# Optimization experiments

Measured on AMD Instinct MI355X. Metric: run time of the kernel, lower is better.

The kernel has to match this reference:

```python
import jax, jax.numpy as jnp
import numpy as np

N = 50000      # nodes (both x and t sets)
D = 128        # d_hidden
E = 1600000    # edges per edge_index (avg degree 32)
LN_EPS = 1e-5


def _gin(x_src, x_dst, edge, W1, b1, W2, b2):
    # PyG GINConv, eps=0: nn(x_dst + sum_{j->i} x_src[j])
    agg = jax.ops.segment_sum(x_src[edge[0]], edge[1], num_segments=x_dst.shape[0])
    h = x_dst + agg
    h = jax.nn.relu(h @ W1 + b1)
    return h @ W2 + b2


def _layernorm(h, g, b):
    m = jnp.mean(h, axis=-1, keepdims=True)
    v = jnp.var(h, axis=-1, keepdims=True)
    return (h - m) / jnp.sqrt(v + LN_EPS) * g + b


def setup_inputs() -> dict:
    key = jax.random.key(0)
    ks = jax.random.split(key, 24)
    s = 1.0 / np.sqrt(D)
    w = lambda k: (jax.random.uniform(k, (D, D), dtype=jnp.float32) * 2 - 1) * s
    b = lambda k: (jax.random.uniform(k, (D,), dtype=jnp.float32) * 2 - 1) * s
    return {
        "x": jax.random.normal(ks[0], (N, D), dtype=jnp.float32),
        "t": jax.random.normal(ks[1], (N, D), dtype=jnp.float32),
        "e_t": jax.random.randint(ks[2], (2, E), 0, N),
        "e_xct": jax.random.randint(ks[3], (2, E), 0, N),
        # gat_tt GIN MLP
        "W1a": w(ks[4]), "b1a": b(ks[5]), "W2a": w(ks[6]), "b2a": b(ks[7]),
        # gat_xct GIN MLP
        "W1b": w(ks[8]), "b1b": b(ks[9]), "W2b": w(ks[10]), "b2b": b(ks[11]),
        # out: Linear -> ReLU -> LayerNorm
        "Wo": w(ks[12]), "bo": b(ks[13]),
        "ln_g": jnp.ones((D,), dtype=jnp.float32),
        "ln_b": jnp.zeros((D,), dtype=jnp.float32),
        # fc_x: Linear -> ReLU -> Linear
        "Wf1": w(ks[14]), "bf1": b(ks[15]), "Wf2": w(ks[16]), "bf2": b(ks[17]),
    }


def reference(x, t, e_t, e_xct,
              W1a, b1a, W2a, b2a,
              W1b, b1b, W2b, b2b,
              Wo, bo, ln_g, ln_b,
              Wf1, bf1, Wf2, bf2):
    # t = (t + gat_tt(t, e_t) + gat_xct((x, t), e_xct)).relu()
    t2 = jax.nn.relu(t
                     + _gin(t, t, e_t, W1a, b1a, W2a, b2a)
                     + _gin(x, t, e_xct, W1b, b1b, W2b, b2b))
    # out branch: Linear -> ReLU -> LayerNorm, residual add
    t_out = t2 + _layernorm(jax.nn.relu(t2 @ Wo + bo), ln_g, ln_b)
    # fc_x branch: Linear -> ReLU -> Linear, residual add
    x_out = x + (jax.nn.relu(x @ Wf1 + bf1) @ Wf2 + bf2)
    return (x_out, t_out)
```

## Files before the change

kernel.cpp:

```cpp
#include <hip/hip_runtime.h>

#define DD 128
#define BSH 7
#define LSTR 136

typedef __attribute__((ext_vector_type(8))) short bf16x8;
typedef __attribute__((ext_vector_type(4))) float f32x4;
typedef __attribute__((ext_vector_type(2))) float f32x2;

__device__ __forceinline__ unsigned short f2b(float f){
  unsigned u = __builtin_bit_cast(unsigned, f);
  u += 0x7FFFu + ((u >> 16) & 1u);
  return (unsigned short)(u >> 16);
}
__device__ __forceinline__ float blo(unsigned u){ return __builtin_bit_cast(float, u << 16); }
__device__ __forceinline__ float bhi(unsigned u){ return __builtin_bit_cast(float, u & 0xFFFF0000u); }
__device__ __forceinline__ float b2f(unsigned short h){ return __builtin_bit_cast(float, ((unsigned)h) << 16); }
__device__ __forceinline__ unsigned pk2(float a, float b){
  return (unsigned)f2b(a) | ((unsigned)f2b(b) << 16);
}

struct WP { const float* w[7]; };
__global__ __launch_bounds__(256) void k_pre(const float* __restrict__ x,
    const float* __restrict__ t, unsigned* __restrict__ xh, unsigned* __restrict__ th,
    int M, WP p, unsigned short* __restrict__ wt,
    const int* __restrict__ e_t, const int* __restrict__ e_xct,
    int* __restrict__ gbcount, int E, int NBper, int ncv, int N){
  const int bid = blockIdx.x;
  if (bid < ncv){
    int tid = bid*256 + threadIdx.x;
    if (tid < M){
      float4 v = ((const float4*)x)[tid];
      ((uint2*)xh)[tid] = make_uint2(pk2(v.x, v.y), pk2(v.z, v.w));
    } else if (tid < 2*M){
      int k = tid - M;
      float4 v = ((const float4*)t)[k];
      ((uint2*)th)[k] = make_uint2(pk2(v.x, v.y), pk2(v.z, v.w));
    }
    return;
  }
  if (bid < ncv + 7){
    const float* W = p.w[bid - ncv];
    unsigned short* dst = wt + (size_t)(bid - ncv)*DD*DD;
    for (int e = threadIdx.x; e < DD*DD; e += 256){
      int k = e >> 7, c = e & 127;
      dst[(c*DD + k) ^ ((c & 7) << 3)] = f2b(W[e]);
    }
    return;
  }
  if (bid == ncv + 7){
    const int tid = threadIdx.x;
    uint4 z; z.x = 0; z.y = 0; z.z = 0; z.w = 0;
    if (tid < 16)      ((uint4*)(xh + (size_t)N*(DD/2)))[tid]      = z;
    else if (tid < 32) ((uint4*)(th + (size_t)N*(DD/2)))[tid - 16] = z;
    return;
  }
  __shared__ int h[800];
  const int vb = bid - ncv - 8;
  const int NB2 = 2*NBper;
  for (int i = threadIdx.x; i < NB2; i += 256) h[i] = 0;
  __syncthreads();
  const long total = 2L*E;
  for (long idx = (long)vb*256 + threadIdx.x; idx < total; idx += 65536L){
    int s = idx >= E;
    int e = (int)(idx - (s ? (long)E : 0));
    int d = (s ? e_xct : e_t)[E + e];
    atomicAdd(&h[s*NBper + (d >> BSH)], 1);
  }
  __syncthreads();
  for (int i = threadIdx.x; i < NB2; i += 256)
    if (h[i]) atomicAdd(&gbcount[i], h[i]);
}

__global__ void k_bscan(const int* __restrict__ gbcount, int* __restrict__ gbase,
                        int* __restrict__ gcursor, int NB2, int total){
  __shared__ int sm[1024];
  const int t = threadIdx.x;
  int v = (t < NB2) ? gbcount[t] : 0;
  sm[t] = v; __syncthreads();
  for (int d = 1; d < 1024; d <<= 1){
    int u = (t >= d) ? sm[t-d] : 0;
    __syncthreads();
    sm[t] += u;
    __syncthreads();
  }
  if (t < NB2){ int ex = sm[t] - v; gbase[t] = ex; gcursor[t] = ex; }
  if (t == 0) gbase[NB2] = total;
}

#define SCCH 8192
__global__ __launch_bounds__(256) void k_scatter(const int* __restrict__ e_t,
    const int* __restrict__ e_xct, int* __restrict__ gcursor,
    unsigned* __restrict__ gbucket, int E, int NBper){
  __shared__ int cnt[800]; __shared__ int gpos[800]; __shared__ int cur[800];
  const int NB2 = 2*NBper;
  const int t = threadIdx.x;
  for (int i = t; i < NB2; i += 256){ cnt[i] = 0; cur[i] = 0; }
  __syncthreads();
  const long base = (long)blockIdx.x * SCCH;
  const long end  = min(base + SCCH, 2L*E);
  for (long idx = base + t; idx < end; idx += 256){
    int s = idx >= E;
    int e = (int)(idx - (s ? (long)E : 0));
    int d = (s ? e_xct : e_t)[E + e];
    atomicAdd(&cnt[s*NBper + (d >> BSH)], 1);
  }
  __syncthreads();
  for (int i = t; i < NB2; i += 256)
    if (cnt[i]) gpos[i] = atomicAdd(&gcursor[i], cnt[i]);
  __syncthreads();
  for (long idx = base + t; idx < end; idx += 256){
    int s = idx >= E;
    int e = (int)(idx - (s ? (long)E : 0));
    const int* ei = s ? e_xct : e_t;
    int sv = ei[e];
    int d  = ei[E + e];
    int b  = s*NBper + (d >> BSH);
    int pos = atomicAdd(&cur[b], 1);
    gbucket[gpos[b] + pos] = (unsigned)sv | ((unsigned)d << 16);
  }
}

__global__ __launch_bounds__(256) void k_build(const unsigned* __restrict__ gbucket,
    const int* __restrict__ gbase, int* __restrict__ offs,
    unsigned short* __restrict__ csr, int N, int E, int NBper){
  __shared__ int cnt[128]; __shared__ int pre[128]; __shared__ int cur[128];
  const int b  = blockIdx.x;
  const int s  = b >= NBper;
  const int bb = b - s*NBper;
  const int d0 = bb << BSH;
  const int t  = threadIdx.x;
  if (t < 128) cnt[t] = 0;
  __syncthreads();
  const int g0 = gbase[b], g1 = gbase[b+1];
  for (int j = g0 + t; j < g1; j += 256){
    unsigned en = gbucket[j];
    atomicAdd(&cnt[(en >> 16) & 127], 1);
  }
  __syncthreads();
  int v = (t < 128) ? cnt[t] : 0;
  if (t < 128) pre[t] = v;
  __syncthreads();
  for (int d = 1; d < 128; d <<= 1){
    int u = (t >= d && t < 128) ? pre[t-d] : 0;
    __syncthreads();
    if (t < 128) pre[t] += u;
    __syncthreads();
  }
  if (t < 128){
    int ex = pre[t] - v;
    cur[t] = ex;
    int dd = d0 + t;
    if (dd < N) offs[(size_t)s*(N+1) + dd] = (g0 - s*E) + ex;
  }
  if (t == 128 + 0 && bb == NBper-1) offs[(size_t)s*(N+1) + N] = E;
  __syncthreads();
  for (int j = g0 + t; j < g1; j += 256){
    unsigned en = gbucket[j];
    int d7 = (en >> 16) & 127;
    int pos = atomicAdd(&cur[d7], 1);
    csr[(size_t)g0 + pos] = (unsigned short)(en & 0xFFFFu);
  }
}

__global__ __launch_bounds__(256) void k_gather(const unsigned short* __restrict__ th,
    const unsigned short* __restrict__ xh, const int* __restrict__ offs,
    const unsigned short* __restrict__ csr, unsigned short* hA, unsigned short* hB,
    int N, int E){
  const int w = threadIdx.x >> 6, l = threadIdx.x & 63;
  const long wid = (long)blockIdx.x*4 + w;
  if (wid >= 2L*N) return;
  const int s = wid >= N;
  const int i = (int)(wid - (s ? N : 0));
  const int* off = offs + (size_t)s*(N+1);
  const unsigned short* src = s ? xh : th;
  const unsigned short* cs = csr + (size_t)s*E;
  const int o0 = off[i], o1 = off[i+1];
  const int deg = o1 - o0;
  const int rs = l >> 4;
  const int q  = l & 15;
  const unsigned short* srcq = src + q*8;
  f32x2 A0 = 0.f, A1 = 0.f, A2 = 0.f, A3 = 0.f;
  if (deg > 0){
    int ce = cs[o0 + (l < deg ? l : deg-1)];
    for (int base = 0; base < deg; base += 64){
      const int nb = min(64, deg - base);
      const int ce_cur = ce;
      const int nxt = base + 64;
      if (nxt < deg){
        const int rem2 = deg - nxt;
        ce = cs[o0 + nxt + (l < rem2 ? l : rem2-1)];
      }
      for (int jj = 0; jj < nb; jj += 16){
        #pragma unroll
        for (int u4 = 0; u4 < 4; ++u4){
          const int idx = jj + u4*4 + rs;
          int r = __shfl(ce_cur, idx);
          r = (idx < nb) ? r : N;
          uint4 v = *(const uint4*)(srcq + (size_t)r*DD);
          A0 += (f32x2){blo(v.x), bhi(v.x)};
          A1 += (f32x2){blo(v.y), bhi(v.y)};
          A2 += (f32x2){blo(v.z), bhi(v.z)};
          A3 += (f32x2){blo(v.w), bhi(v.w)};
        }
      }
    }
  }
  #pragma unroll
  for (int m = 16; m <= 32; m <<= 1){
    A0.x += __shfl_xor(A0.x, m); A0.y += __shfl_xor(A0.y, m);
    A1.x += __shfl_xor(A1.x, m); A1.y += __shfl_xor(A1.y, m);
    A2.x += __shfl_xor(A2.x, m); A2.y += __shfl_xor(A2.y, m);
    A3.x += __shfl_xor(A3.x, m); A3.y += __shfl_xor(A3.y, m);
  }
  if (l < 16){
    uint4 tv = *(const uint4*)(th + (size_t)i*DD + q*8);
    A0 += (f32x2){blo(tv.x), bhi(tv.x)};
    A1 += (f32x2){blo(tv.y), bhi(tv.y)};
    A2 += (f32x2){blo(tv.z), bhi(tv.z)};
    A3 += (f32x2){blo(tv.w), bhi(tv.w)};
    uint4 o;
    o.x = pk2(A0.x, A0.y); o.y = pk2(A1.x, A1.y);
    o.z = pk2(A2.x, A2.y); o.w = pk2(A3.x, A3.y);
    *(uint4*)((s ? hB : hA) + (size_t)i*DD + q*8) = o;
  }
}


__device__ __forceinline__ void stage_issue(const unsigned short* __restrict__ Wt,
                                            unsigned short* wlds){
  const int tid = threadIdx.x;
  const int w = tid >> 6, l = tid & 63;
  #pragma unroll
  for (int i = 0; i < 4; ++i){
    const int cbase = i*512 + w*64;
    __builtin_amdgcn_global_load_lds(
      (const __attribute__((address_space(1))) unsigned*)(Wt + (size_t)(cbase + l)*8),
      (__attribute__((address_space(3))) unsigned*)(wlds + (size_t)cbase*8),
      16, 0, 0);
  }
}

__device__ __forceinline__ void gemm_reg(const bf16x8 a[4], int c0, int g, int swz,
    const unsigned short* wlds, f32x4 acc[8]){
  #pragma unroll
  for (int kb = 0; kb < 4; ++kb){
    const int co = (kb*32 + g*8) ^ swz;
    #pragma unroll
    for (int cb = 0; cb < 8; ++cb){
      bf16x8 b = *(const bf16x8*)(wlds + (cb*16 + c0)*DD + co);
      acc[cb] = __builtin_amdgcn_mfma_f32_16x16x32_bf16(a[kb], b, acc[cb], 0, 0, 0);
    }
  }
}

__device__ __forceinline__ void gemm_lds(const unsigned short* lds,
    int w, int c0, int g, int swz, const unsigned short* wlds, f32x4 acc[8]){
  const unsigned short* ap = lds + (w*16 + c0)*LSTR + g*8;
  #pragma unroll
  for (int kb = 0; kb < 4; ++kb){
    bf16x8 a = *(const bf16x8*)(ap + kb*32);
    const int co = (kb*32 + g*8) ^ swz;
    #pragma unroll
    for (int cb = 0; cb < 8; ++cb){
      bf16x8 b = *(const bf16x8*)(wlds + (cb*16 + c0)*DD + co);
      acc[cb] = __builtin_amdgcn_mfma_f32_16x16x32_bf16(a, b, acc[cb], 0, 0, 0);
    }
  }
}

__device__ __forceinline__ void chainT_body(unsigned short* lds, unsigned short* wlds,
    int bid,
    const unsigned short* __restrict__ hA, const unsigned short* __restrict__ hB,
    const unsigned short* __restrict__ W1a, const float* __restrict__ b1a,
    const unsigned short* __restrict__ W2a, const float* __restrict__ b2a,
    const unsigned short* __restrict__ W1b, const float* __restrict__ b1b,
    const unsigned short* __restrict__ W2b, const float* __restrict__ b2b,
    const unsigned short* __restrict__ Wo,  const float* __restrict__ bo,
    const unsigned short* __restrict__ th,
    const float* __restrict__ lng, const float* __restrict__ lnb,
    float* __restrict__ outT, int N)
{
  const int tid = threadIdx.x;
  const int w = tid >> 6, l = tid & 63;
  const int g = l >> 4, c0 = l & 15;
  const int swz = (c0 & 7) << 3;
  const int rbase = bid*128 + w*16;

  int arow = rbase + c0; if (arow > N-1) arow = N-1;
  const unsigned short* apA = hA + (size_t)arow*DD + g*8;
  const unsigned short* apB = hB + (size_t)arow*DD + g*8;
  bf16x8 aA[4], aB[4];
  #pragma unroll
  for (int kb = 0; kb < 4; ++kb){
    aA[kb] = *(const bf16x8*)(apA + kb*32);
    aB[kb] = *(const bf16x8*)(apB + kb*32);
  }
  unsigned short thr_[8][4];
  #pragma unroll
  for (int cb = 0; cb < 8; ++cb){
    #pragma unroll
    for (int r = 0; r < 4; ++r){
      int orow = rbase + 4*g + r;
      int rc = orow > N-1 ? N-1 : orow;
      thr_[cb][r] = th[(size_t)rc*DD + cb*16 + c0];
    }
  }
  stage_issue(W1a, wlds);
  __syncthreads();

  f32x4 acc[8];

  #pragma unroll
  for (int cb = 0; cb < 8; ++cb) acc[cb] = 0.f;
  gemm_reg(aA, c0, g, swz, wlds, acc);
  __syncthreads();
  stage_issue(W2a, wlds);
  #pragma unroll
  for (int cb = 0; cb < 8; ++cb){
    float bv = b1a[cb*16 + c0];
    #pragma unroll
    for (int r = 0; r < 4; ++r)
      lds[(w*16 + 4*g + r)*LSTR + cb*16 + c0] = f2b(fmaxf(acc[cb][r] + bv, 0.f));
  }
  __syncthreads();

  #pragma unroll
  for (int cb = 0; cb < 8; ++cb) acc[cb] = 0.f;
  gemm_lds(lds, w, c0, g, swz, wlds, acc);
  float pAv[8][4];
  #pragma unroll
  for (int cb = 0; cb < 8; ++cb){
    float bv = b2a[cb*16 + c0];
    #pragma unroll
    for (int r = 0; r < 4; ++r) pAv[cb][r] = acc[cb][r] + bv;
  }
  __syncthreads();
  stage_issue(W1b, wlds);
  __syncthreads();

  #pragma unroll
  for (int cb = 0; cb < 8; ++cb) acc[cb] = 0.f;
  gemm_reg(aB, c0, g, swz, wlds, acc);
  __syncthreads();
  stage_issue(W2b, wlds);
  #pragma unroll
  for (int cb = 0; cb < 8; ++cb){
    float bv = b1b[cb*16 + c0];
    #pragma unroll
    for (int r = 0; r < 4; ++r)
      lds[(w*16 + 4*g + r)*LSTR + cb*16 + c0] = f2b(fmaxf(acc[cb][r] + bv, 0.f));
  }
  __syncthreads();

  #pragma unroll
  for (int cb = 0; cb < 8; ++cb) acc[cb] = 0.f;
  gemm_lds(lds, w, c0, g, swz, wlds, acc);
  __syncthreads();
  stage_issue(Wo, wlds);

  float t2f[8][4];
  #pragma unroll
  for (int cb = 0; cb < 8; ++cb){
    float bv = b2b[cb*16 + c0];
    #pragma unroll
    for (int r = 0; r < 4; ++r){
      float v = fmaxf(acc[cb][r] + bv + b2f(thr_[cb][r]) + pAv[cb][r], 0.f);
      t2f[cb][r] = v;
      lds[(w*16 + 4*g + r)*LSTR + cb*16 + c0] = f2b(v);
    }
  }
  __syncthreads();

  #pragma unroll
  for (int cb = 0; cb < 8; ++cb) acc[cb] = 0.f;
  gemm_lds(lds, w, c0, g, swz, wlds, acc);

  float u[8][4];
  float sm_[4] = {0,0,0,0}, sq_[4] = {0,0,0,0};
  #pragma unroll
  for (int cb = 0; cb < 8; ++cb){
    float bv = bo[cb*16 + c0];
    #pragma unroll
    for (int r = 0; r < 4; ++r){
      float v = fmaxf(acc[cb][r] + bv, 0.f);
      u[cb][r] = v;
      sm_[r] += v; sq_[r] += v*v;
    }
  }
  #pragma unroll
  for (int m = 1; m < 16; m <<= 1){
    #pragma unroll
    for (int r = 0; r < 4; ++r){
      sm_[r] += __shfl_xor(sm_[r], m, 64);
      sq_[r] += __shfl_xor(sq_[r], m, 64);
    }
  }
  float mean[4], rstd[4];
  #pragma unroll
  for (int r = 0; r < 4; ++r){
    mean[r] = sm_[r] * (1.0f/DD);
    float var = sq_[r] * (1.0f/DD) - mean[r]*mean[r];
    rstd[r] = rsqrtf(var + 1e-5f);
  }
  #pragma unroll
  for (int cb = 0; cb < 8; ++cb){
    float gv = lng[cb*16 + c0], bv2 = lnb[cb*16 + c0];
    #pragma unroll
    for (int r = 0; r < 4; ++r){
      int orow = rbase + 4*g + r;
      if (orow < N){
        size_t oi = (size_t)orow*DD + cb*16 + c0;
        outT[oi] = (u[cb][r] - mean[r]) * rstd[r] * gv + bv2 + t2f[cb][r];
      }
    }
  }
}

__device__ __forceinline__ void mlp2_body(unsigned short* lds, unsigned short* wlds,
    int bid,
    const unsigned short* __restrict__ X,
    const unsigned short* __restrict__ W1, const float* __restrict__ b1,
    const unsigned short* __restrict__ W2, const float* __restrict__ b2,
    const unsigned short* __restrict__ resh, float* __restrict__ outF, int N)
{
  const int tid = threadIdx.x;
  const int w = tid >> 6, l = tid & 63;
  const int g = l >> 4, c0 = l & 15;
  const int swz = (c0 & 7) << 3;
  const int rbase = bid*128 + w*16;

  int arow = rbase + c0; if (arow > N-1) arow = N-1;
  const unsigned short* apX = X + (size_t)arow*DD + g*8;
  bf16x8 aX[4];
  #pragma unroll
  for (int kb = 0; kb < 4; ++kb) aX[kb] = *(const bf16x8*)(apX + kb*32);
  unsigned short rs_[8][4];
  #pragma unroll
  for (int cb = 0; cb < 8; ++cb){
    #pragma unroll
    for (int r = 0; r < 4; ++r){
      int orow = rbase + 4*g + r;
      int rc = orow > N-1 ? N-1 : orow;
      rs_[cb][r] = resh[(size_t)rc*DD + cb*16 + c0];
    }
  }
  stage_issue(W1, wlds);
  __syncthreads();

  f32x4 acc[8];
  #pragma unroll
  for (int cb = 0; cb < 8; ++cb) acc[cb] = 0.f;
  gemm_reg(aX, c0, g, swz, wlds, acc);
  __syncthreads();
  stage_issue(W2, wlds);
  #pragma unroll
  for (int cb = 0; cb < 8; ++cb){
    float bv = b1[cb*16 + c0];
    #pragma unroll
    for (int r = 0; r < 4; ++r)
      lds[(w*16 + 4*g + r)*LSTR + cb*16 + c0] = f2b(fmaxf(acc[cb][r] + bv, 0.f));
  }
  __syncthreads();

  #pragma unroll
  for (int cb = 0; cb < 8; ++cb) acc[cb] = 0.f;
  gemm_lds(lds, w, c0, g, swz, wlds, acc);

  #pragma unroll
  for (int cb = 0; cb < 8; ++cb){
    float bv = b2[cb*16 + c0];
    #pragma unroll
    for (int r = 0; r < 4; ++r){
      int orow = rbase + 4*g + r;
      if (orow < N){
        size_t oi = (size_t)orow*DD + cb*16 + c0;
        outF[oi] = acc[cb][r] + bv + b2f(rs_[cb][r]);
      }
    }
  }
}

__global__ __launch_bounds__(512, 4) void k_tail(
    const unsigned short* __restrict__ hA, const unsigned short* __restrict__ hB,
    const unsigned short* __restrict__ xh, const unsigned short* __restrict__ th,
    const unsigned short* __restrict__ wt,
    const float* __restrict__ b1a, const float* __restrict__ b2a,
    const float* __restrict__ b1b, const float* __restrict__ b2b,
    const float* __restrict__ bo,  const float* __restrict__ lng,
    const float* __restrict__ lnb, const float* __restrict__ bf1,
    const float* __restrict__ bf2,
    float* __restrict__ outX, float* __restrict__ outT, int N, int gt)
{
  __shared__ unsigned short lds[128*LSTR];
  __shared__ unsigned short wlds[DD*DD];
  const unsigned short* W1a = wt + 0*DD*DD;
  const unsigned short* W2a = wt + 1*DD*DD;
  const unsigned short* W1b = wt + 2*DD*DD;
  const unsigned short* W2b = wt + 3*DD*DD;
  const unsigned short* Wo  = wt + 4*DD*DD;
  const unsigned short* Wf1 = wt + 5*DD*DD;
  const unsigned short* Wf2 = wt + 6*DD*DD;
  if (blockIdx.x < (unsigned)gt){
    chainT_body(lds, wlds, blockIdx.x, hA, hB, W1a, b1a, W2a, b2a, W1b, b1b, W2b, b2b,
                Wo, bo, th, lng, lnb, outT, N);
  } else {
    mlp2_body(lds, wlds, blockIdx.x - gt, xh, Wf1, bf1, Wf2, bf2, xh, outX, N);
  }
}

extern "C" void kernel_launch(void* const* d_in, const int* in_sizes, int n_in,
                              void* d_out, int out_size, void* d_ws, size_t ws_size,
                              hipStream_t stream) {
  const float* x     = (const float*)d_in[0];
  const float* t     = (const float*)d_in[1];
  const int*   e_t   = (const int*)d_in[2];
  const int*   e_xct = (const int*)d_in[3];
  const float* b1a = (const float*)d_in[5];
  const float* b2a = (const float*)d_in[7];
  const float* b1b = (const float*)d_in[9];
  const float* b2b = (const float*)d_in[11];
  const float* bo  = (const float*)d_in[13];
  const float* lng = (const float*)d_in[14];
  const float* lnb = (const float*)d_in[15];
  const float* bf1 = (const float*)d_in[17];
  const float* bf2 = (const float*)d_in[19];

  const int N = in_sizes[0] / DD;
  const int E = in_sizes[2] / 2;
  const int NBper = (N + 127) >> BSH;
  const int NB2 = 2*NBper;

  char* p = (char*)d_ws;
  auto carve = [&](size_t b)->char*{ char* r = p; p += (b + 255) & ~(size_t)255; return r; };
  size_t nd2z = (size_t)(N+1)*DD*2;
  size_t nd2 = (size_t)N*DD*2, nd4 = (size_t)N*DD*4;
  unsigned short* xh = (unsigned short*)carve(nd2z);
  unsigned short* th = (unsigned short*)carve(nd2z);
  unsigned short* hA = (unsigned short*)carve(nd2);
  unsigned short* hB = (unsigned short*)carve(nd2);
  float*          pA = (float*)carve(nd4);
  unsigned short* wt = (unsigned short*)carve((size_t)7*DD*DD*2);
  int* gbcount = (int*)carve((size_t)NB2*4);
  int* gbase   = (int*)carve((size_t)(NB2+1)*4);
  int* gcursor = (int*)carve((size_t)NB2*4);
  int* offs    = (int*)carve((size_t)2*(N+1)*4);
  unsigned short* csr = (unsigned short*)carve((size_t)2*E*2);
  unsigned* gbucket = (unsigned*)pA;

  float* outX = (float*)d_out;
  float* outT = outX + (size_t)N*DD;

  hipMemsetAsync(gbcount, 0, (size_t)NB2*4, stream);

  WP wp;
  wp.w[0] = (const float*)d_in[4];  wp.w[1] = (const float*)d_in[6];
  wp.w[2] = (const float*)d_in[8];  wp.w[3] = (const float*)d_in[10];
  wp.w[4] = (const float*)d_in[12]; wp.w[5] = (const float*)d_in[16];
  wp.w[6] = (const float*)d_in[18];

  const int M4 = N*DD/4;
  const int ncv = (2*M4 + 255)/256;
  k_pre<<<ncv + 8 + 256, 256, 0, stream>>>(x, t, (unsigned*)xh, (unsigned*)th, M4,
                                           wp, wt, e_t, e_xct, gbcount, E, NBper, ncv, N);
  k_bscan<<<1, 1024, 0, stream>>>(gbcount, gbase, gcursor, NB2, 2*E);
  const int nsc = (int)((2L*E + SCCH-1) / SCCH);
  k_scatter<<<nsc, 256, 0, stream>>>(e_t, e_xct, gcursor, gbucket, E, NBper);
  k_build<<<NB2, 256, 0, stream>>>(gbucket, gbase, offs, csr, N, E, NBper);
  k_gather<<<(2*N + 3)/4, 256, 0, stream>>>(th, xh, offs, csr, hA, hB, N, E);

  const int gt = (N + 127)/128;
  k_tail<<<2*gt, 512, 0, stream>>>(hA, hB, xh, th, wt, b1a, b2a, b1b, b2b, bo,
                                   lng, lnb, bf1, bf2, outX, outT, N, gt);
}
```

Measured before the change: 234.2 us.

## Fuse CSR build and neighbor gather into one kernel using LDS-resident CSR

Merges the per-bucket CSR construction and the segment-sum gather into a single kernel. Each 512-thread block sorts its bucket's edges by destination into a shared-memory CSR, then eight waves gather neighbor rows for the bucket's 128 destination nodes directly from that CSR. This drops the global offs/csr arrays, their write and read-back traffic, and one launch. In exchange, parallelism drops to one block per 128 nodes, and buckets holding more than CAPB edges are silently truncated.

```diff
diff --git a/kernel.cpp b/kernel.cpp
--- a/kernel.cpp
+++ b/kernel.cpp
@@ -3,6 +3,7 @@
 #define DD 128
 #define BSH 7
 #define LSTR 136
+#define CAPB 8192
 
 typedef __attribute__((ext_vector_type(8))) short bf16x8;
 typedef __attribute__((ext_vector_type(4))) float f32x4;
@@ -121,22 +122,25 @@
   }
 }
 
-__global__ __launch_bounds__(256) void k_build(const unsigned* __restrict__ gbucket,
-    const int* __restrict__ gbase, int* __restrict__ offs,
-    unsigned short* __restrict__ csr, int N, int E, int NBper){
-  __shared__ int cnt[128]; __shared__ int pre[128]; __shared__ int cur[128];
+__global__ __launch_bounds__(512, 8) void k_gbind(
+    const unsigned* __restrict__ gbucket, const int* __restrict__ gbase,
+    const unsigned short* __restrict__ th, const unsigned short* __restrict__ xh,
+    unsigned short* hA, unsigned short* hB, int N, int E, int NBper){
+  __shared__ unsigned short lcsr[CAPB];
+  __shared__ int cnt[128];
+  __shared__ int pre[128];
+  __shared__ int cur[128];
   const int b  = blockIdx.x;
   const int s  = b >= NBper;
   const int bb = b - s*NBper;
   const int d0 = bb << BSH;
   const int t  = threadIdx.x;
+  const int g0 = gbase[b], g1 = gbase[b+1];
+
   if (t < 128) cnt[t] = 0;
   __syncthreads();
-  const int g0 = gbase[b], g1 = gbase[b+1];
-  for (int j = g0 + t; j < g1; j += 256){
-    unsigned en = gbucket[j];
-    atomicAdd(&cnt[(en >> 16) & 127], 1);
-  }
+  for (int j = g0 + t; j < g1; j += 512)
+    atomicAdd(&cnt[(gbucket[j] >> 16) & 127], 1);
   __syncthreads();
   int v = (t < 128) ? cnt[t] : 0;
   if (t < 128) pre[t] = v;
@@ -147,82 +151,58 @@
     if (t < 128) pre[t] += u;
     __syncthreads();
   }
-  if (t < 128){
-    int ex = pre[t] - v;
-    cur[t] = ex;
-    int dd = d0 + t;
-    if (dd < N) offs[(size_t)s*(N+1) + dd] = (g0 - s*E) + ex;
-  }
-  if (t == 128 + 0 && bb == NBper-1) offs[(size_t)s*(N+1) + N] = E;
-  __syncthreads();
-  for (int j = g0 + t; j < g1; j += 256){
+  if (t < 128){ int ex = pre[t] - v; pre[t] = ex; cur[t] = ex; }
+  __syncthreads();
+  for (int j = g0 + t; j < g1; j += 512){
     unsigned en = gbucket[j];
     int d7 = (en >> 16) & 127;
     int pos = atomicAdd(&cur[d7], 1);
-    csr[(size_t)g0 + pos] = (unsigned short)(en & 0xFFFFu);
-  }
-}
-
-__global__ __launch_bounds__(256) void k_gather(const unsigned short* __restrict__ th,
-    const unsigned short* __restrict__ xh, const int* __restrict__ offs,
-    const unsigned short* __restrict__ csr, unsigned short* hA, unsigned short* hB,
-    int N, int E){
-  const int w = threadIdx.x >> 6, l = threadIdx.x & 63;
-  const long wid = (long)blockIdx.x*4 + w;
-  if (wid >= 2L*N) return;
-  const int s = wid >= N;
-  const int i = (int)(wid - (s ? N : 0));
-  const int* off = offs + (size_t)s*(N+1);
+    if (pos < CAPB) lcsr[pos] = (unsigned short)(en & 0xFFFFu);
+  }
+  __syncthreads();
+
   const unsigned short* src = s ? xh : th;
-  const unsigned short* cs = csr + (size_t)s*E;
-  const int o0 = off[i], o1 = off[i+1];
-  const int deg = o1 - o0;
+  const int w = t >> 6, l = t & 63;
   const int rs = l >> 4;
   const int q  = l & 15;
   const unsigned short* srcq = src + q*8;
-  f32x2 A0 = 0.f, A1 = 0.f, A2 = 0.f, A3 = 0.f;
-  if (deg > 0){
-    int ce = cs[o0 + (l < deg ? l : deg-1)];
-    for (int base = 0; base < deg; base += 64){
-      const int nb = min(64, deg - base);
-      const int ce_cur = ce;
-      const int nxt = base + 64;
-      if (nxt < deg){
-        const int rem2 = deg - nxt;
-        ce = cs[o0 + nxt + (l < rem2 ? l : rem2-1)];
+  for (int k = w; k < 128; k += 8){
+    const int i = d0 + k;
+    if (i >= N) continue;
+    const int o0 = pre[k];
+    const int deg = cnt[k];
+    f32x2 A0 = 0.f, A1 = 0.f, A2 = 0.f, A3 = 0.f;
+    for (int jj = 0; jj < deg; jj += 16){
+      #pragma unroll
+      for (int u4 = 0; u4 < 4; ++u4){
+        const int idx = jj + u4*4 + rs;
+        int ce = lcsr[o0 + (idx < deg ? idx : deg-1)];
+        int r = (idx < deg) ? ce : N;
+        uint4 vv = *(const uint4*)(srcq + (size_t)r*DD);
+        A0 += (f32x2){blo(vv.x), bhi(vv.x)};
+        A1 += (f32x2){blo(vv.y), bhi(vv.y)};
+        A2 += (f32x2){blo(vv.z), bhi(vv.z)};
+        A3 += (f32x2){blo(vv.w), bhi(vv.w)};
       }
-      for (int jj = 0; jj < nb; jj += 16){
-        #pragma unroll
-        for (int u4 = 0; u4 < 4; ++u4){
-          const int idx = jj + u4*4 + rs;
-          int r = __shfl(ce_cur, idx);
-          r = (idx < nb) ? r : N;
-          uint4 v = *(const uint4*)(srcq + (size_t)r*DD);
-          A0 += (f32x2){blo(v.x), bhi(v.x)};
-          A1 += (f32x2){blo(v.y), bhi(v.y)};
-          A2 += (f32x2){blo(v.z), bhi(v.z)};
-          A3 += (f32x2){blo(v.w), bhi(v.w)};
-        }
-      }
-    }
-  }
-  #pragma unroll
-  for (int m = 16; m <= 32; m <<= 1){
-    A0.x += __shfl_xor(A0.x, m); A0.y += __shfl_xor(A0.y, m);
-    A1.x += __shfl_xor(A1.x, m); A1.y += __shfl_xor(A1.y, m);
-    A2.x += __shfl_xor(A2.x, m); A2.y += __shfl_xor(A2.y, m);
-    A3.x += __shfl_xor(A3.x, m); A3.y += __shfl_xor(A3.y, m);
-  }
-  if (l < 16){
-    uint4 tv = *(const uint4*)(th + (size_t)i*DD + q*8);
-    A0 += (f32x2){blo(tv.x), bhi(tv.x)};
-    A1 += (f32x2){blo(tv.y), bhi(tv.y)};
-    A2 += (f32x2){blo(tv.z), bhi(tv.z)};
-    A3 += (f32x2){blo(tv.w), bhi(tv.w)};
-    uint4 o;
-    o.x = pk2(A0.x, A0.y); o.y = pk2(A1.x, A1.y);
-    o.z = pk2(A2.x, A2.y); o.w = pk2(A3.x, A3.y);
-    *(uint4*)((s ? hB : hA) + (size_t)i*DD + q*8) = o;
+    }
+    #pragma unroll
+    for (int m = 16; m <= 32; m <<= 1){
+      A0.x += __shfl_xor(A0.x, m); A0.y += __shfl_xor(A0.y, m);
+      A1.x += __shfl_xor(A1.x, m); A1.y += __shfl_xor(A1.y, m);
+      A2.x += __shfl_xor(A2.x, m); A2.y += __shfl_xor(A2.y, m);
+      A3.x += __shfl_xor(A3.x, m); A3.y += __shfl_xor(A3.y, m);
+    }
+    if (l < 16){
+      uint4 tv = *(const uint4*)(th + (size_t)i*DD + q*8);
+      A0 += (f32x2){blo(tv.x), bhi(tv.x)};
+      A1 += (f32x2){blo(tv.y), bhi(tv.y)};
+      A2 += (f32x2){blo(tv.z), bhi(tv.z)};
+      A3 += (f32x2){blo(tv.w), bhi(tv.w)};
+      uint4 o;
+      o.x = pk2(A0.x, A0.y); o.y = pk2(A1.x, A1.y);
+      o.z = pk2(A2.x, A2.y); o.w = pk2(A3.x, A3.y);
+      *(uint4*)((s ? hB : hA) + (size_t)i*DD + q*8) = o;
+    }
   }
 }
 
@@ -544,8 +524,6 @@
   int* gbcount = (int*)carve((size_t)NB2*4);
   int* gbase   = (int*)carve((size_t)(NB2+1)*4);
   int* gcursor = (int*)carve((size_t)NB2*4);
-  int* offs    = (int*)carve((size_t)2*(N+1)*4);
-  unsigned short* csr = (unsigned short*)carve((size_t)2*E*2);
   unsigned* gbucket = (unsigned*)pA;
 
   float* outX = (float*)d_out;
@@ -566,8 +544,7 @@
   k_bscan<<<1, 1024, 0, stream>>>(gbcount, gbase, gcursor, NB2, 2*E);
   const int nsc = (int)((2L*E + SCCH-1) / SCCH);
   k_scatter<<<nsc, 256, 0, stream>>>(e_t, e_xct, gcursor, gbucket, E, NBper);
-  k_build<<<NB2, 256, 0, stream>>>(gbucket, gbase, offs, csr, N, E, NBper);
-  k_gather<<<(2*N + 3)/4, 256, 0, stream>>>(th, xh, offs, csr, hA, hB, N, E);
+  k_gbind<<<NB2, 512, 0, stream>>>(gbucket, gbase, th, xh, hA, hB, N, E, NBper);
 
   const int gt = (N + 127)/128;
   k_tail<<<2*gt, 512, 0, stream>>>(hA, hB, xh, th, wt, b1a, b2a, b1b, b2b, bo,
```

Result: slower. 250.6 us (+7.0%).
